# Performance work log

Measured on AMD Instinct MI355X. Metric: run time of the kernel, lower is better.

Reference implementation:

```python
import jax, jax.numpy as jnp
import numpy as np

N = 10000       # nodes (= number of eigenpairs)
NFEAT = 512
NCLASS = 64     # hidden size of attention/FFN when norm='none'
HID = 128       # feat_encoder hidden
DIM = 32        # eig encoder hidden_dim
K = 10          # outer loop count of ParamNonHarmonicEncoding
NF = DIM // 2   # num_freq = 16
OMEGA = 50.0
DMIN = 0.25
NLAYER = 1


def _ln(x, g, b, eps=1e-5):
    m = jnp.mean(x, axis=-1, keepdims=True)
    v = jnp.mean((x - m) ** 2, axis=-1, keepdims=True)
    return g * (x - m) / jnp.sqrt(v + eps) + b


def setup_inputs() -> dict:
    key = jax.random.key(0)
    ks = jax.random.split(key, 32)
    f32 = jnp.float32
    def w(k, shape, s=0.05):
        return jax.random.normal(k, shape, dtype=f32) * s
    inp = {
        "e": jax.random.uniform(ks[0], (N,), dtype=f32),
        "u": jax.random.normal(ks[1], (N, N), dtype=f32) / np.float32(np.sqrt(N)),
        "x": jax.random.normal(ks[2], (N, NFEAT), dtype=f32),
        # feat_encoder: Linear(nfeat,hid) -> ReLU -> Linear(hid,nclass)
        "fe_w1": w(ks[3], (NFEAT, HID)), "fe_b1": jnp.zeros((HID,), f32),
        "fe_w2": w(ks[4], (HID, NCLASS)), "fe_b2": jnp.zeros((NCLASS,), f32),
        # ParamNonHarmonicEncoding
        "freq_deltas": jax.random.uniform(ks[5], (NF,), dtype=f32) * 0.5,
        "freq_bias": jnp.zeros((), f32),
        "readout_w": w(ks[6], (K, 1 + 2 * NF), 0.1),
        "readout_b": jnp.zeros((K,), f32),
        "alpha_w": w(ks[7], (K, 1), 0.3),   # nn.Linear(k,1,bias=False)
        # mha pre-norm
        "mha_ln_g": jnp.ones((NCLASS,), f32), "mha_ln_b": jnp.zeros((NCLASS,), f32),
        # Diff attention (H=1, hidden=nclass)
        "wq1": w(ks[8], (NCLASS, NCLASS)), "bq1": jnp.zeros((NCLASS,), f32),
        "wk1": w(ks[9], (NCLASS, NCLASS)), "bk1": jnp.zeros((NCLASS,), f32),
        "wq2": w(ks[10], (NCLASS, NCLASS)), "bq2": jnp.zeros((NCLASS,), f32),
        "wk2": w(ks[11], (NCLASS, NCLASS)), "bk2": jnp.zeros((NCLASS,), f32),
        "wv": w(ks[12], (NCLASS, NCLASS)), "bv": jnp.zeros((NCLASS,), f32),
        "lq1": w(ks[13], (NCLASS,), 0.1), "lk1": w(ks[14], (NCLASS,), 0.1),
        "lq2": w(ks[15], (NCLASS,), 0.1), "lk2": w(ks[16], (NCLASS,), 0.1),
        "attn_ln_g": jnp.ones((NCLASS,), f32), "attn_ln_b": jnp.zeros((NCLASS,), f32),
        "out_w": w(ks[17], (NCLASS, NCLASS)), "out_b": jnp.zeros((NCLASS,), f32),
        # gating
        "gate_ln_g": jnp.ones((3 * NCLASS,), f32), "gate_ln_b": jnp.zeros((3 * NCLASS,), f32),
        "gate_w": w(ks[18], (3 * NCLASS, 3)), "gate_b": jnp.zeros((3,), f32),
        # FFN
        "ffn_ln_g": jnp.ones((NCLASS,), f32), "ffn_ln_b": jnp.zeros((NCLASS,), f32),
        "ffn_w1": w(ks[19], (NCLASS, NCLASS)), "ffn_b1": jnp.zeros((NCLASS,), f32),
        "ffn_w2": w(ks[20], (NCLASS, NCLASS)), "ffn_b2": jnp.zeros((NCLASS,), f32),
    }
    return inp


def reference(e, u, x, fe_w1, fe_b1, fe_w2, fe_b2,
              freq_deltas, freq_bias, readout_w, readout_b, alpha_w,
              mha_ln_g, mha_ln_b,
              wq1, bq1, wk1, bk1, wq2, bq2, wk2, bk2, wv, bv,
              lq1, lk1, lq2, lk2, attn_ln_g, attn_ln_b, out_w, out_b,
              gate_ln_g, gate_ln_b, gate_w, gate_b,
              ffn_ln_g, ffn_ln_b, ffn_w1, ffn_b1, ffn_w2, ffn_b2):
    # feat encoder (all dropouts are 0 / eval mode)
    h = jnp.maximum(x @ fe_w1 + fe_b1, 0.0) @ fe_w2 + fe_b2          # [N, C]

    # ParamNonHarmonicEncoding, vectorized over the k powers
    deltas = jax.nn.softplus(freq_deltas) + DMIN
    freqs = jnp.cumsum(deltas) + freq_bias
    freqs = OMEGA * jnp.tanh(freqs / OMEGA)                           # [F]
    powers = e[:, None] ** jnp.arange(1, K + 1, dtype=e.dtype)        # [N, K]
    phase = powers[:, :, None] * freqs                                # [N, K, F]
    ns = jnp.asarray(NF ** 0.5, e.dtype)
    feat = jnp.concatenate(
        [jnp.ones_like(powers)[..., None], jnp.sin(phase) / ns, jnp.cos(phase) / ns],
        axis=-1)                                                      # [N, K, 1+2F]
    eig = jnp.einsum('nkf,kf->nk', feat, readout_w) + readout_b      # [N, K]
    new_e = eig @ alpha_w                                             # [N, 1]

    for layer in range(NLAYER):
        # spectral propagation: u @ diag-like(new_e) @ u^T @ h
        utx = u.T @ h                                                 # [N, C]
        h_fur = u @ (new_e * utx)                                     # [N, C]

        # differential linear attention
        mh = _ln(h, mha_ln_g, mha_ln_b)
        q1 = mh @ wq1 + bq1; k1 = mh @ wk1 + bk1
        q2 = mh @ wq2 + bq2; k2 = mh @ wk2 + bk2
        v = mh @ wv + bv
        k1v = k1.T @ v                                                # [C, C]
        k2v = k2.T @ v
        lam1 = jnp.exp(jnp.sum(lq1 * lk1))
        lam2 = jnp.exp(jnp.sum(lq2 * lk2))
        lam_init = 0.8 - 0.6 * float(np.exp(-0.3 * layer))
        lam_full = lam1 - lam2 + lam_init
        xa = q1 @ k1v - (q2 @ k2v) * lam_full
        xa = _ln(xa, attn_ln_g, attn_ln_b) * (1.0 - lam_init)
        mha_h = xa @ out_w + out_b                                    # [N, C]

        # gated mixing
        cat = jnp.concatenate([h, mha_h, h_fur], axis=-1)             # [N, 3C]
        g = jax.nn.softmax(_ln(cat, gate_ln_g, gate_ln_b) @ gate_w + gate_b, axis=-1)
        mix = h * g[:, 0:1] + mha_h * g[:, 1:2] + h_fur * g[:, 2:3]

        f = _ln(mix, ffn_ln_g, ffn_ln_b)
        f = jax.nn.gelu(f @ ffn_w1 + ffn_b1, approximate=False) @ ffn_w2 + ffn_b2
        h = mix + f
    return h
```

## Files before the change

### kernel.cpp

```cpp
#include <hip/hip_runtime.h>
#include <hip/hip_bf16.h>
#include <math.h>

#define NN 10000
#define J48 10048
#define CHUNKS 157
#define CPS 20
#define SPLITS 8

typedef __bf16 bf16;
typedef bf16 bf16x8 __attribute__((ext_vector_type(8)));
typedef float f32x4 __attribute__((ext_vector_type(4)));

__device__ __forceinline__ float wave_sum64(float v) {
#pragma unroll
  for (int m = 32; m >= 1; m >>= 1) v += __shfl_xor(v, m, 64);
  return v;
}

__global__ void prep_kernel(const float* __restrict__ w1, const float* __restrict__ w2,
                            const float* __restrict__ wq1, const float* __restrict__ wk1,
                            const float* __restrict__ wq2, const float* __restrict__ wk2,
                            const float* __restrict__ wvw,
                            const float* __restrict__ bq1, const float* __restrict__ bk1,
                            const float* __restrict__ bq2, const float* __restrict__ bk2,
                            const float* __restrict__ bvv,
                            const float* __restrict__ lq1, const float* __restrict__ lk1,
                            const float* __restrict__ lq2, const float* __restrict__ lk2,
                            const float* __restrict__ freq_deltas, const float* __restrict__ freq_bias,
                            bf16* __restrict__ w1T, bf16* __restrict__ w2T, bf16* __restrict__ qkvT,
                            float* __restrict__ bqkv, float* __restrict__ freqs, float* __restrict__ lamb) {
  int tid = blockIdx.x * blockDim.x + threadIdx.x;
  int nthr = gridDim.x * blockDim.x;
  for (int i = tid; i < 512 * 128; i += nthr) {
    int o = i >> 9, k = i & 511;
    w1T[i] = (bf16)w1[k * 128 + o];
  }
  for (int i = tid; i < 64 * 128; i += nthr) {
    int o = i >> 7, k = i & 127;
    w2T[i] = (bf16)w2[k * 64 + o];
  }
  for (int i = tid; i < 320 * 64; i += nthr) {
    int r = i >> 6, k = i & 63;
    const float* W = (r < 64) ? wq1 : (r < 128) ? wk1 : (r < 192) ? wq2 : (r < 256) ? wk2 : wvw;
    qkvT[i] = (bf16)W[k * 64 + (r & 63)];
  }
  for (int i = tid; i < 320; i += nthr) {
    const float* B = (i < 64) ? bq1 : (i < 128) ? bk1 : (i < 192) ? bq2 : (i < 256) ? bk2 : bvv;
    bqkv[i] = B[i & 63];
  }
  if (blockIdx.x == 0) {
    if (threadIdx.x == 0) {
      float acc = freq_bias[0];
      for (int f = 0; f < 16; f++) {
        acc += log1pf(expf(freq_deltas[f])) + 0.25f;
        freqs[f] = 50.0f * tanhf(acc * (1.0f / 50.0f));
      }
    }
    if (threadIdx.x >= 64 && threadIdx.x < 128) {
      int l = threadIdx.x - 64;
      float s1 = wave_sum64(lq1[l] * lk1[l]);
      float s2 = wave_sum64(lq2[l] * lk2[l]);
      if (l == 0) lamb[0] = expf(s1) - expf(s2) + 0.2f;
    }
  }
}

__global__ void newe_kernel(const float* __restrict__ e, const float* __restrict__ rw,
                            const float* __restrict__ rb, const float* __restrict__ aw,
                            const float* __restrict__ freqs, float* __restrict__ newe) {
  int n = blockIdx.x * blockDim.x + threadIdx.x;
  if (n >= NN) return;
  float fr[16];
#pragma unroll
  for (int f = 0; f < 16; f++) fr[f] = freqs[f];
  float ev = e[n], p = 1.0f, acc = 0.0f;
  for (int k = 0; k < 10; k++) {
    p *= ev;
    float s = rb[k] + rw[k * 33];
#pragma unroll
    for (int f = 0; f < 16; f++) {
      float ph = p * fr[f];
      s += 0.25f * (__sinf(ph) * rw[k * 33 + 1 + f] + __cosf(ph) * rw[k * 33 + 17 + f]);
    }
    acc += s * aw[k];
  }
  newe[n] = acc;
}

__global__ __launch_bounds__(256) void ucopy_kernel(const float* __restrict__ u, bf16* __restrict__ ubf) {
  size_t base = ((size_t)blockIdx.x * 256 + threadIdx.x) * 8;
  size_t stride = (size_t)gridDim.x * 256 * 8;
  for (size_t i = base; i < (size_t)NN * NN; i += stride) {
    float4 a = *(const float4*)(u + i);
    float4 b = *(const float4*)(u + i + 4);
    union { uint4 v; bf16 h[8]; } pk;
    pk.h[0] = (bf16)a.x; pk.h[1] = (bf16)a.y; pk.h[2] = (bf16)a.z; pk.h[3] = (bf16)a.w;
    pk.h[4] = (bf16)b.x; pk.h[5] = (bf16)b.y; pk.h[6] = (bf16)b.z; pk.h[7] = (bf16)b.w;
    *(uint4*)(ubf + i) = pk.v;
  }
}

__global__ __launch_bounds__(256) void g1_kernel(const float* __restrict__ x, const bf16* __restrict__ w1T,
                                                 const float* __restrict__ b1, bf16* __restrict__ t1b) {
  __shared__ bf16 la[64][40];
  __shared__ bf16 lb[128][40];
  const int bm = blockIdx.x * 64;
  const int lane = threadIdx.x & 63, wvid = threadIdx.x >> 6;
  const int am = threadIdx.x >> 2, aseg = (threadIdx.x & 3) * 8;
  const int arow = bm + am;
  f32x4 acc[8] = {};
  float4 aLo, aHi;
  uint4 bChunk[2];
  auto fetchAll = [&](int k0) {
    if (arow < NN) {
      const float4* p = (const float4*)(x + (size_t)arow * 512 + k0 + aseg);
      aLo = p[0]; aHi = p[1];
    } else {
      aLo = make_float4(0.f, 0.f, 0.f, 0.f); aHi = aLo;
    }
#pragma unroll
    for (int r = 0; r < 2; r++) {
      int slot = threadIdx.x * 2 + r;
      int n = slot >> 2, seg = (slot & 3) * 8;
      bChunk[r] = *(const uint4*)(w1T + n * 512 + k0 + seg);
    }
  };
  auto store = [&]() {
    union { uint4 v; bf16 b[8]; } pk;
    float av[8] = {aLo.x, aLo.y, aLo.z, aLo.w, aHi.x, aHi.y, aHi.z, aHi.w};
#pragma unroll
    for (int t = 0; t < 8; t++) pk.b[t] = (bf16)av[t];
    *(uint4*)&la[am][aseg] = pk.v;
#pragma unroll
    for (int r = 0; r < 2; r++) {
      int slot = threadIdx.x * 2 + r;
      int n = slot >> 2, seg = (slot & 3) * 8;
      *(uint4*)&lb[n][seg] = bChunk[r];
    }
  };
  fetchAll(0);
  for (int k0 = 0; k0 < 512; k0 += 32) {
    store();
    if (k0 + 32 < 512) fetchAll(k0 + 32);
    __syncthreads();
    bf16x8 af = *(const bf16x8*)&la[wvid * 16 + (lane & 15)][(lane >> 4) * 8];
#pragma unroll
    for (int s = 0; s < 8; s++) {
      bf16x8 bfr = *(const bf16x8*)&lb[s * 16 + (lane & 15)][(lane >> 4) * 8];
      acc[s] = __builtin_amdgcn_mfma_f32_16x16x32_bf16(af, bfr, acc[s], 0, 0, 0);
    }
    __syncthreads();
  }
#pragma unroll
  for (int s = 0; s < 8; s++) {
    int col = s * 16 + (lane & 15);
    float bvv = b1[col];
#pragma unroll
    for (int r = 0; r < 4; r++) {
      int row = bm + wvid * 16 + (lane >> 4) * 4 + r;
      if (row < NN) {
        float v = acc[s][r] + bvv;
        t1b[(size_t)row * 128 + col] = (bf16)(v > 0.f ? v : 0.f);
      }
    }
  }
}

__global__ __launch_bounds__(256) void g2_kernel(const bf16* __restrict__ t1b, const bf16* __restrict__ w2T,
                                                 const float* __restrict__ b2, const float* __restrict__ lng,
                                                 const float* __restrict__ lnb, float* __restrict__ h,
                                                 bf16* __restrict__ hT, bf16* __restrict__ mh) {
  __shared__ bf16 la[64][72];
  __shared__ bf16 lb[64][72];
  const int bm = blockIdx.x * 64;
  const int lane = threadIdx.x & 63, wvid = threadIdx.x >> 6;
  f32x4 acc[4] = {};
  for (int k0 = 0; k0 < 128; k0 += 64) {
#pragma unroll
    for (int r = 0; r < 2; r++) {
      int slot = threadIdx.x * 2 + r;
      int m = slot >> 3, seg = (slot & 7) * 8;
      int row = bm + m;
      uint4 val = make_uint4(0u, 0u, 0u, 0u);
      if (row < NN) val = *(const uint4*)(t1b + (size_t)row * 128 + k0 + seg);
      *(uint4*)&la[m][seg] = val;
      *(uint4*)&lb[m][seg] = *(const uint4*)(w2T + m * 128 + k0 + seg);
    }
    __syncthreads();
#pragma unroll
    for (int ks = 0; ks < 2; ks++) {
      bf16x8 af = *(const bf16x8*)&la[wvid * 16 + (lane & 15)][ks * 32 + (lane >> 4) * 8];
#pragma unroll
      for (int s = 0; s < 4; s++) {
        bf16x8 bfr = *(const bf16x8*)&lb[s * 16 + (lane & 15)][ks * 32 + (lane >> 4) * 8];
        acc[s] = __builtin_amdgcn_mfma_f32_16x16x32_bf16(af, bfr, acc[s], 0, 0, 0);
      }
    }
    __syncthreads();
  }
  float bv4[4], g4[4], lb4[4];
#pragma unroll
  for (int s = 0; s < 4; s++) {
    int col = s * 16 + (lane & 15);
    bv4[s] = b2[col]; g4[s] = lng[col]; lb4[s] = lnb[col];
  }
#pragma unroll
  for (int r = 0; r < 4; r++) {
    float vals[4], psum = 0.f;
#pragma unroll
    for (int s = 0; s < 4; s++) { vals[s] = acc[s][r] + bv4[s]; psum += vals[s]; }
#pragma unroll
    for (int msk = 1; msk < 16; msk <<= 1) psum += __shfl_xor(psum, msk, 64);
    float mean = psum * (1.0f / 64.0f);
    float pvar = 0.f;
#pragma unroll
    for (int s = 0; s < 4; s++) { float dd = vals[s] - mean; pvar += dd * dd; }
#pragma unroll
    for (int msk = 1; msk < 16; msk <<= 1) pvar += __shfl_xor(pvar, msk, 64);
    float rsq = rsqrtf(pvar * (1.0f / 64.0f) + 1e-5f);
    int row = bm + wvid * 16 + (lane >> 4) * 4 + r;
    if (row < NN) {
#pragma unroll
      for (int s = 0; s < 4; s++) {
        int col = s * 16 + (lane & 15);
        float v = vals[s];
        h[(size_t)row * 64 + col] = v;
        hT[(size_t)col * NN + row] = (bf16)v;
        mh[(size_t)row * 64 + col] = (bf16)(g4[s] * (v - mean) * rsq + lb4[s]);
      }
    }
  }
}

__global__ __launch_bounds__(256) void qkv_kernel(const bf16* __restrict__ mh, const bf16* __restrict__ qkvT,
                                                  const float* __restrict__ bqkv,
                                                  bf16* __restrict__ qq, bf16* __restrict__ kv) {
  __shared__ bf16 la[64][72];
  __shared__ bf16 lb[320][72];
  const int bm = blockIdx.x * 64;
  const int lane = threadIdx.x & 63, wvid = threadIdx.x >> 6;
#pragma unroll
  for (int r = 0; r < 2; r++) {
    int slot = threadIdx.x * 2 + r;
    int m = slot >> 3, seg = (slot & 7) * 8;
    int row = bm + m;
    uint4 val = make_uint4(0u, 0u, 0u, 0u);
    if (row < NN) val = *(const uint4*)(mh + (size_t)row * 64 + seg);
    *(uint4*)&la[m][seg] = val;
  }
#pragma unroll
  for (int r = 0; r < 10; r++) {
    int slot = threadIdx.x * 10 + r;
    int n = slot >> 3, seg = (slot & 7) * 8;
    *(uint4*)&lb[n][seg] = *(const uint4*)(qkvT + n * 64 + seg);
  }
  __syncthreads();
  f32x4 acc[20] = {};
#pragma unroll
  for (int ks = 0; ks < 2; ks++) {
    bf16x8 af = *(const bf16x8*)&la[wvid * 16 + (lane & 15)][ks * 32 + (lane >> 4) * 8];
#pragma unroll
    for (int s = 0; s < 20; s++) {
      bf16x8 bfr = *(const bf16x8*)&lb[s * 16 + (lane & 15)][ks * 32 + (lane >> 4) * 8];
      acc[s] = __builtin_amdgcn_mfma_f32_16x16x32_bf16(af, bfr, acc[s], 0, 0, 0);
    }
  }
#pragma unroll
  for (int s = 0; s < 20; s++) {
    int col = s * 16 + (lane & 15);
    float bvv = bqkv[col];
    bf16* dst; int dc, stride;
    if (col < 64)       { dst = qq; dc = col;       stride = 128; }
    else if (col < 128) { dst = kv; dc = col - 64;  stride = 192; }
    else if (col < 192) { dst = qq; dc = col - 64;  stride = 128; }
    else                { dst = kv; dc = col - 128; stride = 192; }
#pragma unroll
    for (int r = 0; r < 4; r++) {
      int row = bm + wvid * 16 + (lane >> 4) * 4 + r;
      if (row < NN) dst[(size_t)row * stride + dc] = (bf16)(acc[s][r] + bvv);
    }
  }
}

__global__ __launch_bounds__(256) void r1_kernel(const bf16* __restrict__ kv, float* __restrict__ part) {
  int b = blockIdx.x;
  int c1 = threadIdx.x & 63, grp = threadIdx.x >> 6;
  int r0 = b * 16;
  float a1[16] = {}, a2[16] = {};
  for (int r = 0; r < 16; r++) {
    const bf16* rowp = kv + (size_t)(r0 + r) * 192;
    float k1 = (float)rowp[c1];
    float k2 = (float)rowp[64 + c1];
    union { uint4 v; bf16 b[8]; } v0, v1;
    v0.v = *(const uint4*)(rowp + 128 + grp * 16);
    v1.v = *(const uint4*)(rowp + 136 + grp * 16);
#pragma unroll
    for (int q = 0; q < 8; q++) {
      float va = (float)v0.b[q], vb = (float)v1.b[q];
      a1[q] += k1 * va; a2[q] += k2 * va;
      a1[8 + q] += k1 * vb; a2[8 + q] += k2 * vb;
    }
  }
  float* p1 = part + (size_t)b * 8192 + (size_t)c1 * 64 + grp * 16;
  float* p2 = p1 + 4096;
#pragma unroll
  for (int q = 0; q < 16; q++) { p1[q] = a1[q]; p2[q] = a2[q]; }
}

__global__ __launch_bounds__(256) void r2a_kernel(const float* __restrict__ part, float* __restrict__ part2) {
  int flat = blockIdx.x * 256 + threadIdx.x;
  int y = blockIdx.y;
  int b0 = y * 79, b1 = min(625, b0 + 79);
  float s = 0.f;
  for (int b = b0; b < b1; b++) s += part[(size_t)b * 8192 + flat];
  part2[(size_t)flat * 8 + y] = s;
}

__global__ void r2b_kernel(const float* __restrict__ part2, const float* __restrict__ lamb, bf16* __restrict__ Bt) {
  int flat = blockIdx.x * 256 + threadIdx.x;
  int mat = flat >> 12, rem = flat & 4095;
  int d = rem >> 6, c = rem & 63;
  f32x4 lo = *(const f32x4*)(part2 + (size_t)flat * 8);
  f32x4 hi = *(const f32x4*)(part2 + (size_t)flat * 8 + 4);
  float s = lo[0] + lo[1] + lo[2] + lo[3] + hi[0] + hi[1] + hi[2] + hi[3];
  float v = mat ? (-lamb[0] * s) : s;
  Bt[c * 128 + mat * 64 + d] = (bf16)v;
}

__global__ __launch_bounds__(256) void d_split_kernel(const bf16* __restrict__ ubf, const bf16* __restrict__ hT,
                                                      float* __restrict__ dpart) {
  __shared__ bf16 la[64][72];
  __shared__ bf16 lb[64][72];
  const int j0 = blockIdx.x * 64;
  const int sk = blockIdx.y;
  const int c0 = sk * CPS, c1e = min(CHUNKS, c0 + CPS);
  const int t = threadIdx.x;
  const int lane = t & 63, wv = t >> 6;
  const int jl = (t & 15) * 4;
  const int ir = (t >> 4) * 4;
  f32x4 acc[4] = {};
  uint4 aC[2];
  uint2 uc[4];
  auto fetchAll = [&](int i0) {
#pragma unroll
    for (int r = 0; r < 2; r++) {
      int slot = t * 2 + r;
      int c = slot >> 3, seg = (slot & 7) * 8;
      int i = i0 + seg;
      if (i + 7 < NN) aC[r] = *(const uint4*)(hT + (size_t)c * NN + i);
      else {
        union { uint4 v; bf16 b[8]; } tu;
#pragma unroll
        for (int q = 0; q < 8; q++) tu.b[q] = (i + q < NN) ? hT[(size_t)c * NN + i + q] : (bf16)0.f;
        aC[r] = tu.v;
      }
    }
#pragma unroll
    for (int q = 0; q < 4; q++) {
      int i = i0 + ir + q;
      if (i < NN && (j0 + jl + 3) < NN) uc[q] = *(const uint2*)(ubf + (size_t)i * NN + j0 + jl);
      else if (i < NN) {
        union { uint2 w; bf16 b[4]; } tu;
#pragma unroll
        for (int q2 = 0; q2 < 4; q2++) tu.b[q2] = (j0 + jl + q2 < NN) ? ubf[(size_t)i * NN + j0 + jl + q2] : (bf16)0.f;
        uc[q] = tu.w;
      } else uc[q] = make_uint2(0u, 0u);
    }
  };
  auto storeAll = [&]() {
#pragma unroll
    for (int r = 0; r < 2; r++) {
      int slot = t * 2 + r;
      int c = slot >> 3, seg = (slot & 7) * 8;
      *(uint4*)&la[c][seg] = aC[r];
    }
#pragma unroll
    for (int q2 = 0; q2 < 4; q2++) {
      int j = jl + q2;
      int isw = ir ^ (((j >> 2) & 3) << 3);
      union { uint2 w; bf16 b[4]; } pk;
      pk.b[0] = ((const bf16*)&uc[0])[q2];
      pk.b[1] = ((const bf16*)&uc[1])[q2];
      pk.b[2] = ((const bf16*)&uc[2])[q2];
      pk.b[3] = ((const bf16*)&uc[3])[q2];
      *(uint2*)&lb[j][isw] = pk.w;
    }
  };
  fetchAll(c0 * 64);
  for (int ch = c0; ch < c1e; ch++) {
    storeAll();
    if (ch + 1 < c1e) fetchAll((ch + 1) * 64);
    __syncthreads();
#pragma unroll
    for (int ks = 0; ks < 2; ks++) {
      bf16x8 af = *(const bf16x8*)&la[wv * 16 + (lane & 15)][ks * 32 + (lane >> 4) * 8];
#pragma unroll
      for (int s = 0; s < 4; s++) {
        int j = s * 16 + (lane & 15);
        int ioff = (ks * 32 + (lane >> 4) * 8) ^ (((j >> 2) & 3) << 3);
        bf16x8 bfr = *(const bf16x8*)&lb[j][ioff];
        acc[s] = __builtin_amdgcn_mfma_f32_16x16x32_bf16(af, bfr, acc[s], 0, 0, 0);
      }
    }
    __syncthreads();
  }
#pragma unroll
  for (int s = 0; s < 4; s++) {
    int j = j0 + s * 16 + (lane & 15);
#pragma unroll
    for (int r = 0; r < 4; r++) {
      int c = wv * 16 + (lane >> 4) * 4 + r;
      dpart[((size_t)sk * 64 + c) * J48 + j] = acc[s][r];
    }
  }
}

__global__ void dred_kernel(const float* __restrict__ dpart, const float* __restrict__ newe,
                            bf16* __restrict__ wutxT) {
  int idx = blockIdx.x * 256 + threadIdx.x;
  int c = idx / 2512;
  int j = (idx - c * 2512) * 4;
  if (c >= 64 || j >= NN) return;
  f32x4 s = {};
  for (int sk = 0; sk < SPLITS; sk++)
    s += *(const f32x4*)(dpart + ((size_t)sk * 64 + c) * J48 + j);
  union { uint2 w; bf16 b[4]; } pk;
#pragma unroll
  for (int q = 0; q < 4; q++) pk.b[q] = (bf16)(newe[j + q] * s[q]);
  *(uint2*)&wutxT[(size_t)c * NN + j] = pk.w;
}

__global__ __launch_bounds__(256) void e_split_kernel(const bf16* __restrict__ ubf, const bf16* __restrict__ wutxT,
                                                      float* __restrict__ epart) {
  __shared__ bf16 la[64][72];
  __shared__ bf16 lb[64][72];
  const int bm = blockIdx.x * 64;
  const int sk = blockIdx.y;
  const int c0 = sk * CPS, c1e = min(CHUNKS, c0 + CPS);
  const int t = threadIdx.x;
  const int lane = t & 63, wv = t >> 6;
  const int mA = t >> 2, segA = (t & 3) * 16;
  const int mrow = bm + mA;
  f32x4 acc[4] = {};
  uint4 aU[2];
  uint4 bC[2];
  auto fetchAll = [&](int j0) {
    int j = j0 + segA;
    if (mrow < NN && j + 15 < NN) {
      aU[0] = *(const uint4*)(ubf + (size_t)mrow * NN + j);
      aU[1] = *(const uint4*)(ubf + (size_t)mrow * NN + j + 8);
    } else {
      union { uint4 v[2]; bf16 b[16]; } tu;
#pragma unroll
      for (int q = 0; q < 16; q++)
        tu.b[q] = (mrow < NN && j + q < NN) ? ubf[(size_t)mrow * NN + j + q] : (bf16)0.f;
      aU[0] = tu.v[0]; aU[1] = tu.v[1];
    }
#pragma unroll
    for (int r = 0; r < 2; r++) {
      int slot = t * 2 + r;
      int c = slot >> 3, seg = (slot & 7) * 8;
      int jj = j0 + seg;
      if (jj + 7 < NN) bC[r] = *(const uint4*)(wutxT + (size_t)c * NN + jj);
      else {
        union { uint4 v; bf16 b[8]; } tu;
#pragma unroll
        for (int q = 0; q < 8; q++) tu.b[q] = (jj + q < NN) ? wutxT[(size_t)c * NN + jj + q] : (bf16)0.f;
        bC[r] = tu.v;
      }
    }
  };
  auto storeAll = [&]() {
    *(uint4*)&la[mA][segA] = aU[0];
    *(uint4*)&la[mA][segA + 8] = aU[1];
#pragma unroll
    for (int r = 0; r < 2; r++) {
      int slot = t * 2 + r;
      int c = slot >> 3, seg = (slot & 7) * 8;
      *(uint4*)&lb[c][seg] = bC[r];
    }
  };
  fetchAll(c0 * 64);
  for (int ch = c0; ch < c1e; ch++) {
    storeAll();
    if (ch + 1 < c1e) fetchAll((ch + 1) * 64);
    __syncthreads();
#pragma unroll
    for (int ks = 0; ks < 2; ks++) {
      bf16x8 af = *(const bf16x8*)&la[wv * 16 + (lane & 15)][ks * 32 + (lane >> 4) * 8];
#pragma unroll
      for (int s = 0; s < 4; s++) {
        bf16x8 bfr = *(const bf16x8*)&lb[s * 16 + (lane & 15)][ks * 32 + (lane >> 4) * 8];
        acc[s] = __builtin_amdgcn_mfma_f32_16x16x32_bf16(af, bfr, acc[s], 0, 0, 0);
      }
    }
    __syncthreads();
  }
#pragma unroll
  for (int s = 0; s < 4; s++) {
    int col = s * 16 + (lane & 15);
#pragma unroll
    for (int r = 0; r < 4; r++) {
      int row = wv * 16 + (lane >> 4) * 4 + r;
      epart[((size_t)sk * J48 + bm + row) * 64 + col] = acc[s][r];
    }
  }
}

__global__ void ered_kernel(const float* __restrict__ epart, float* __restrict__ h_fur) {
  int idx = blockIdx.x * 256 + threadIdx.x;
  if (idx >= NN * 16) return;
  size_t off = (size_t)idx * 4;
  f32x4 s = {};
  for (int sk = 0; sk < SPLITS; sk++)
    s += *(const f32x4*)(epart + (size_t)sk * (J48 * 64) + off);
  *(f32x4*)(h_fur + off) = s;
}

__global__ __launch_bounds__(256) void hattn_kernel(const bf16* __restrict__ qq, const bf16* __restrict__ Bt,
                                                    const float* __restrict__ g, const float* __restrict__ b,
                                                    bf16* __restrict__ xan) {
  __shared__ bf16 la[64][136];
  __shared__ bf16 lb[64][136];
  const int bm = blockIdx.x * 64;
  const int lane = threadIdx.x & 63, wvid = threadIdx.x >> 6;
#pragma unroll
  for (int r = 0; r < 4; r++) {
    int slot = threadIdx.x * 4 + r;
    int m = slot >> 4, seg = (slot & 15) * 8;
    int row = bm + m;
    uint4 val = make_uint4(0u, 0u, 0u, 0u);
    if (row < NN) val = *(const uint4*)(qq + (size_t)row * 128 + seg);
    *(uint4*)&la[m][seg] = val;
    *(uint4*)&lb[m][seg] = *(const uint4*)(Bt + m * 128 + seg);
  }
  __syncthreads();
  f32x4 acc[4] = {};
#pragma unroll
  for (int ks = 0; ks < 4; ks++) {
    bf16x8 af = *(const bf16x8*)&la[wvid * 16 + (lane & 15)][ks * 32 + (lane >> 4) * 8];
#pragma unroll
    for (int s = 0; s < 4; s++) {
      bf16x8 bfr = *(const bf16x8*)&lb[s * 16 + (lane & 15)][ks * 32 + (lane >> 4) * 8];
      acc[s] = __builtin_amdgcn_mfma_f32_16x16x32_bf16(af, bfr, acc[s], 0, 0, 0);
    }
  }
#pragma unroll
  for (int r = 0; r < 4; r++) {
    float psum = acc[0][r] + acc[1][r] + acc[2][r] + acc[3][r];
#pragma unroll
    for (int msk = 1; msk < 16; msk <<= 1) psum += __shfl_xor(psum, msk, 64);
    float mean = psum * (1.0f / 64.0f);
    float pvar = 0.f;
#pragma unroll
    for (int s = 0; s < 4; s++) { float dd = acc[s][r] - mean; pvar += dd * dd; }
#pragma unroll
    for (int msk = 1; msk < 16; msk <<= 1) pvar += __shfl_xor(pvar, msk, 64);
    float rsq = rsqrtf(pvar * (1.0f / 64.0f) + 1e-5f);
    int row = bm + wvid * 16 + (lane >> 4) * 4 + r;
    if (row < NN) {
#pragma unroll
      for (int s = 0; s < 4; s++) {
        int col = s * 16 + (lane & 15);
        float o = 0.8f * (g[col] * (acc[s][r] - mean) * rsq + b[col]);
        xan[(size_t)row * 64 + col] = (bf16)o;
      }
    }
  }
}

__global__ __launch_bounds__(256) void final_kernel(const float* __restrict__ h, const float* __restrict__ h_fur,
                                                    const bf16* __restrict__ xan,
                                                    const float* __restrict__ out_w, const float* __restrict__ out_b,
                                                    const float* __restrict__ gg, const float* __restrict__ gb,
                                                    const float* __restrict__ gw, const float* __restrict__ gbias,
                                                    const float* __restrict__ fg, const float* __restrict__ fb,
                                                    const float* __restrict__ fw1, const float* __restrict__ fb1,
                                                    const float* __restrict__ fw2, const float* __restrict__ fb2,
                                                    float* __restrict__ out) {
  __shared__ float s_ow[64][64];
  __shared__ float s_w1[64][64];
  __shared__ float s_w2[64][64];
  __shared__ float s_gw[192][3];
  __shared__ float s_row[4][64];
  const int lane = threadIdx.x & 63, wvid = threadIdx.x >> 6;
  for (int i = threadIdx.x; i < 4096; i += 256) {
    ((float*)s_ow)[i] = out_w[i];
    ((float*)s_w1)[i] = fw1[i];
    ((float*)s_w2)[i] = fw2[i];
  }
  for (int i = threadIdx.x; i < 576; i += 256) ((float*)s_gw)[i] = gw[i];
  const int row = blockIdx.x * 4 + wvid;
  float x_h = h[(size_t)row * 64 + lane];
  float x_f = h_fur[(size_t)row * 64 + lane];
  float x_a = (float)xan[(size_t)row * 64 + lane];
  s_row[wvid][lane] = x_a;
  __syncthreads();
  float mha = out_b[lane];
#pragma unroll 8
  for (int d = 0; d < 64; d++) mha += s_row[wvid][d] * s_ow[d][lane];
  float m3 = wave_sum64(x_h + mha + x_f) * (1.0f / 192.0f);
  float dh = x_h - m3, dm = mha - m3, df = x_f - m3;
  float v3 = wave_sum64(dh * dh + dm * dm + df * df) * (1.0f / 192.0f);
  float rs3 = rsqrtf(v3 + 1e-5f);
  float l0 = gg[lane] * dh * rs3 + gb[lane];
  float l1 = gg[64 + lane] * dm * rs3 + gb[64 + lane];
  float l2 = gg[128 + lane] * df * rs3 + gb[128 + lane];
  float p0 = l0 * s_gw[lane][0] + l1 * s_gw[64 + lane][0] + l2 * s_gw[128 + lane][0];
  float p1 = l0 * s_gw[lane][1] + l1 * s_gw[64 + lane][1] + l2 * s_gw[128 + lane][1];
  float p2 = l0 * s_gw[lane][2] + l1 * s_gw[64 + lane][2] + l2 * s_gw[128 + lane][2];
  p0 = wave_sum64(p0) + gbias[0];
  p1 = wave_sum64(p1) + gbias[1];
  p2 = wave_sum64(p2) + gbias[2];
  float mx = fmaxf(p0, fmaxf(p1, p2));
  float e0 = expf(p0 - mx), e1 = expf(p1 - mx), e2 = expf(p2 - mx);
  float inv = 1.0f / (e0 + e1 + e2);
  float mix = x_h * (e0 * inv) + mha * (e1 * inv) + x_f * (e2 * inv);
  float mf = wave_sum64(mix) * (1.0f / 64.0f);
  float dmx = mix - mf;
  float vf = wave_sum64(dmx * dmx) * (1.0f / 64.0f);
  float f = fg[lane] * dmx * rsqrtf(vf + 1e-5f) + fb[lane];
  __syncthreads();
  s_row[wvid][lane] = f;
  __syncthreads();
  float t1 = fb1[lane];
#pragma unroll 8
  for (int d = 0; d < 64; d++) t1 += s_row[wvid][d] * s_w1[d][lane];
  t1 = 0.5f * t1 * (1.0f + erff(t1 * 0.70710678118654752f));
  __syncthreads();
  s_row[wvid][lane] = t1;
  __syncthreads();
  float f2 = fb2[lane];
#pragma unroll 8
  for (int d = 0; d < 64; d++) f2 += s_row[wvid][d] * s_w2[d][lane];
  out[(size_t)row * 64 + lane] = mix + f2;
}

extern "C" void kernel_launch(void* const* d_in, const int* in_sizes, int n_in,
                              void* d_out, int out_size, void* d_ws, size_t ws_size,
                              hipStream_t stream) {
  const float* e          = (const float*)d_in[0];
  const float* u          = (const float*)d_in[1];
  const float* x          = (const float*)d_in[2];
  const float* fe_w1      = (const float*)d_in[3];
  const float* fe_b1      = (const float*)d_in[4];
  const float* fe_w2      = (const float*)d_in[5];
  const float* fe_b2      = (const float*)d_in[6];
  const float* freq_deltas= (const float*)d_in[7];
  const float* freq_bias  = (const float*)d_in[8];
  const float* readout_w  = (const float*)d_in[9];
  const float* readout_b  = (const float*)d_in[10];
  const float* alpha_w    = (const float*)d_in[11];
  const float* mha_ln_g   = (const float*)d_in[12];
  const float* mha_ln_b   = (const float*)d_in[13];
  const float* wq1        = (const float*)d_in[14];
  const float* bq1        = (const float*)d_in[15];
  const float* wk1        = (const float*)d_in[16];
  const float* bk1        = (const float*)d_in[17];
  const float* wq2        = (const float*)d_in[18];
  const float* bq2        = (const float*)d_in[19];
  const float* wk2        = (const float*)d_in[20];
  const float* bk2        = (const float*)d_in[21];
  const float* wv_in      = (const float*)d_in[22];
  const float* bv_in      = (const float*)d_in[23];
  const float* lq1        = (const float*)d_in[24];
  const float* lk1        = (const float*)d_in[25];
  const float* lq2        = (const float*)d_in[26];
  const float* lk2        = (const float*)d_in[27];
  const float* attn_ln_g  = (const float*)d_in[28];
  const float* attn_ln_b  = (const float*)d_in[29];
  const float* out_w      = (const float*)d_in[30];
  const float* out_b      = (const float*)d_in[31];
  const float* gate_ln_g  = (const float*)d_in[32];
  const float* gate_ln_b  = (const float*)d_in[33];
  const float* gate_w     = (const float*)d_in[34];
  const float* gate_b     = (const float*)d_in[35];
  const float* ffn_ln_g   = (const float*)d_in[36];
  const float* ffn_ln_b   = (const float*)d_in[37];
  const float* ffn_w1     = (const float*)d_in[38];
  const float* ffn_b1     = (const float*)d_in[39];
  const float* ffn_w2     = (const float*)d_in[40];
  const float* ffn_b2     = (const float*)d_in[41];

  constexpr size_t OFF_H     = 0;
  constexpr size_t OFF_T1B   = 2560000;
  constexpr size_t OFF_HT    = 5120000;
  constexpr size_t OFF_MH    = 6400000;
  constexpr size_t OFF_QQ    = 7680000;
  constexpr size_t OFF_KV    = 10240000;
  constexpr size_t OFF_WUTXT = 14080000;
  constexpr size_t OFF_HFUR  = 15360000;
  constexpr size_t OFF_XAN   = 17920000;
  constexpr size_t OFF_NEWE  = 19200000;
  constexpr size_t OFF_BT    = 19240064;
  constexpr size_t OFF_W1T   = 19256448;
  constexpr size_t OFF_W2T   = 19387520;
  constexpr size_t OFF_QKVT  = 19403904;
  constexpr size_t OFF_BQKV  = 19444864;
  constexpr size_t OFF_FREQS = 19446144;
  constexpr size_t OFF_LAM   = 19446208;
  constexpr size_t OFF_BIG   = 19446272;
  constexpr size_t SZ_SPART  = (size_t)SPLITS * 64 * J48 * 4;
  constexpr size_t OFF_PART2 = OFF_BIG + SZ_SPART;
  constexpr size_t OFF_UBF   = OFF_PART2 + 262144;
  constexpr size_t WS_NEED   = OFF_UBF + (size_t)NN * NN * 2;
  if (ws_size < WS_NEED) return;

  char* ws = (char*)d_ws;
  float* h_buf   = (float*)(ws + OFF_H);
  bf16*  t1b     = (bf16*)(ws + OFF_T1B);
  bf16*  hT      = (bf16*)(ws + OFF_HT);
  bf16*  mh      = (bf16*)(ws + OFF_MH);
  bf16*  qq      = (bf16*)(ws + OFF_QQ);
  bf16*  kv      = (bf16*)(ws + OFF_KV);
  bf16*  wutxT   = (bf16*)(ws + OFF_WUTXT);
  float* h_fur   = (float*)(ws + OFF_HFUR);
  bf16*  xan     = (bf16*)(ws + OFF_XAN);
  float* newe    = (float*)(ws + OFF_NEWE);
  bf16*  Bt      = (bf16*)(ws + OFF_BT);
  bf16*  w1T     = (bf16*)(ws + OFF_W1T);
  bf16*  w2T     = (bf16*)(ws + OFF_W2T);
  bf16*  qkvT    = (bf16*)(ws + OFF_QKVT);
  float* bqkv    = (float*)(ws + OFF_BQKV);
  float* freqs   = (float*)(ws + OFF_FREQS);
  float* lamb    = (float*)(ws + OFF_LAM);
  float* part    = (float*)(ws + OFF_BIG);
  float* part2   = (float*)(ws + OFF_PART2);
  float* dpart   = (float*)(ws + OFF_BIG);
  float* epart   = (float*)(ws + OFF_BIG);
  bf16*  ubf     = (bf16*)(ws + OFF_UBF);

  prep_kernel<<<64, 256, 0, stream>>>(fe_w1, fe_w2, wq1, wk1, wq2, wk2, wv_in,
                                      bq1, bk1, bq2, bk2, bv_in,
                                      lq1, lk1, lq2, lk2, freq_deltas, freq_bias,
                                      w1T, w2T, qkvT, bqkv, freqs, lamb);
  newe_kernel<<<40, 256, 0, stream>>>(e, readout_w, readout_b, alpha_w, freqs, newe);
  g1_kernel<<<157, 256, 0, stream>>>(x, w1T, fe_b1, t1b);
  g2_kernel<<<157, 256, 0, stream>>>(t1b, w2T, fe_b2, mha_ln_g, mha_ln_b, h_buf, hT, mh);
  qkv_kernel<<<157, 256, 0, stream>>>(mh, qkvT, bqkv, qq, kv);
  r1_kernel<<<625, 256, 0, stream>>>(kv, part);
  r2a_kernel<<<dim3(32, 8), 256, 0, stream>>>(part, part2);
  r2b_kernel<<<32, 256, 0, stream>>>(part2, lamb, Bt);
  ucopy_kernel<<<2048, 256, 0, stream>>>(u, ubf);
  d_split_kernel<<<dim3(157, SPLITS), 256, 0, stream>>>(ubf, hT, dpart);
  dred_kernel<<<628, 256, 0, stream>>>(dpart, newe, wutxT);
  e_split_kernel<<<dim3(157, SPLITS), 256, 0, stream>>>(ubf, wutxT, epart);
  ered_kernel<<<625, 256, 0, stream>>>(epart, h_fur);
  hattn_kernel<<<157, 256, 0, stream>>>(qq, Bt, attn_ln_g, attn_ln_b, xan);
  final_kernel<<<2500, 256, 0, stream>>>(h_buf, h_fur, xan, out_w, out_b,
                                         gate_ln_g, gate_ln_b, gate_w, gate_b,
                                         ffn_ln_g, ffn_ln_b, ffn_w1, ffn_b1, ffn_w2, ffn_b2,
                                         (float*)d_out);
}
```

Baseline: 405.5 us.

## Fuse fp32-to-bf16 conversion of u into split GEMM loads and relax barriers

Removes the separate pass that converts the 10000x10000 eigenvector matrix to bf16. The two split GEMM kernels now read fp32 u directly and convert it while staging to LDS. This removes one full write plus reread of the bf16 copy and one launch, but doubles the bytes each GEMM reads. The block barriers now wait only on LDS counters, so global prefetches can stay in flight across the barrier.

```diff
diff --git a/kernel.cpp b/kernel.cpp
--- a/kernel.cpp
+++ b/kernel.cpp
@@ -11,6 +11,13 @@
 typedef __bf16 bf16;
 typedef bf16 bf16x8 __attribute__((ext_vector_type(8)));
 typedef float f32x4 __attribute__((ext_vector_type(4)));
+
+#define SYNC_LDS() do {                                      \
+    asm volatile("s_waitcnt lgkmcnt(0)" ::: "memory");       \
+    __builtin_amdgcn_sched_barrier(0);                       \
+    __builtin_amdgcn_s_barrier();                            \
+    __builtin_amdgcn_sched_barrier(0);                       \
+  } while (0)
 
 __device__ __forceinline__ float wave_sum64(float v) {
 #pragma unroll
@@ -88,19 +95,6 @@
   newe[n] = acc;
 }
 
-__global__ __launch_bounds__(256) void ucopy_kernel(const float* __restrict__ u, bf16* __restrict__ ubf) {
-  size_t base = ((size_t)blockIdx.x * 256 + threadIdx.x) * 8;
-  size_t stride = (size_t)gridDim.x * 256 * 8;
-  for (size_t i = base; i < (size_t)NN * NN; i += stride) {
-    float4 a = *(const float4*)(u + i);
-    float4 b = *(const float4*)(u + i + 4);
-    union { uint4 v; bf16 h[8]; } pk;
-    pk.h[0] = (bf16)a.x; pk.h[1] = (bf16)a.y; pk.h[2] = (bf16)a.z; pk.h[3] = (bf16)a.w;
-    pk.h[4] = (bf16)b.x; pk.h[5] = (bf16)b.y; pk.h[6] = (bf16)b.z; pk.h[7] = (bf16)b.w;
-    *(uint4*)(ubf + i) = pk.v;
-  }
-}
-
 __global__ __launch_bounds__(256) void g1_kernel(const float* __restrict__ x, const bf16* __restrict__ w1T,
                                                  const float* __restrict__ b1, bf16* __restrict__ t1b) {
   __shared__ bf16 la[64][40];
@@ -328,7 +322,7 @@
   Bt[c * 128 + mat * 64 + d] = (bf16)v;
 }
 
-__global__ __launch_bounds__(256) void d_split_kernel(const bf16* __restrict__ ubf, const bf16* __restrict__ hT,
+__global__ __launch_bounds__(256) void d_split_kernel(const float* __restrict__ u, const bf16* __restrict__ hT,
                                                       float* __restrict__ dpart) {
   __shared__ bf16 la[64][72];
   __shared__ bf16 lb[64][72];
@@ -341,7 +335,7 @@
   const int ir = (t >> 4) * 4;
   f32x4 acc[4] = {};
   uint4 aC[2];
-  uint2 uc[4];
+  float4 bC[4];
   auto fetchAll = [&](int i0) {
 #pragma unroll
     for (int r = 0; r < 2; r++) {
@@ -359,13 +353,13 @@
 #pragma unroll
     for (int q = 0; q < 4; q++) {
       int i = i0 + ir + q;
-      if (i < NN && (j0 + jl + 3) < NN) uc[q] = *(const uint2*)(ubf + (size_t)i * NN + j0 + jl);
+      if (i < NN && (j0 + jl + 3) < NN) bC[q] = *(const float4*)(u + (size_t)i * NN + j0 + jl);
       else if (i < NN) {
-        union { uint2 w; bf16 b[4]; } tu;
-#pragma unroll
-        for (int q2 = 0; q2 < 4; q2++) tu.b[q2] = (j0 + jl + q2 < NN) ? ubf[(size_t)i * NN + j0 + jl + q2] : (bf16)0.f;
-        uc[q] = tu.w;
-      } else uc[q] = make_uint2(0u, 0u);
+        float tmp[4];
+#pragma unroll
+        for (int q2 = 0; q2 < 4; q2++) tmp[q2] = (j0 + jl + q2 < NN) ? u[(size_t)i * NN + j0 + jl + q2] : 0.f;
+        bC[q] = make_float4(tmp[0], tmp[1], tmp[2], tmp[3]);
+      } else bC[q] = make_float4(0.f, 0.f, 0.f, 0.f);
     }
   };
   auto storeAll = [&]() {
@@ -380,10 +374,10 @@
       int j = jl + q2;
       int isw = ir ^ (((j >> 2) & 3) << 3);
       union { uint2 w; bf16 b[4]; } pk;
-      pk.b[0] = ((const bf16*)&uc[0])[q2];
-      pk.b[1] = ((const bf16*)&uc[1])[q2];
-      pk.b[2] = ((const bf16*)&uc[2])[q2];
-      pk.b[3] = ((const bf16*)&uc[3])[q2];
+      pk.b[0] = (bf16)((float*)&bC[0])[q2];
+      pk.b[1] = (bf16)((float*)&bC[1])[q2];
+      pk.b[2] = (bf16)((float*)&bC[2])[q2];
+      pk.b[3] = (bf16)((float*)&bC[3])[q2];
       *(uint2*)&lb[j][isw] = pk.w;
     }
   };
@@ -391,7 +385,7 @@
   for (int ch = c0; ch < c1e; ch++) {
     storeAll();
     if (ch + 1 < c1e) fetchAll((ch + 1) * 64);
-    __syncthreads();
+    SYNC_LDS();
 #pragma unroll
     for (int ks = 0; ks < 2; ks++) {
       bf16x8 af = *(const bf16x8*)&la[wv * 16 + (lane & 15)][ks * 32 + (lane >> 4) * 8];
@@ -403,7 +397,7 @@
         acc[s] = __builtin_amdgcn_mfma_f32_16x16x32_bf16(af, bfr, acc[s], 0, 0, 0);
       }
     }
-    __syncthreads();
+    SYNC_LDS();
   }
 #pragma unroll
   for (int s = 0; s < 4; s++) {
@@ -431,7 +425,7 @@
   *(uint2*)&wutxT[(size_t)c * NN + j] = pk.w;
 }
 
-__global__ __launch_bounds__(256) void e_split_kernel(const bf16* __restrict__ ubf, const bf16* __restrict__ wutxT,
+__global__ __launch_bounds__(256) void e_split_kernel(const float* __restrict__ u, const bf16* __restrict__ wutxT,
                                                       float* __restrict__ epart) {
   __shared__ bf16 la[64][72];
   __shared__ bf16 lb[64][72];
@@ -443,19 +437,24 @@
   const int mA = t >> 2, segA = (t & 3) * 16;
   const int mrow = bm + mA;
   f32x4 acc[4] = {};
-  uint4 aU[2];
+  float4 aC[4];
   uint4 bC[2];
   auto fetchAll = [&](int j0) {
     int j = j0 + segA;
     if (mrow < NN && j + 15 < NN) {
-      aU[0] = *(const uint4*)(ubf + (size_t)mrow * NN + j);
-      aU[1] = *(const uint4*)(ubf + (size_t)mrow * NN + j + 8);
+      const float4* p = (const float4*)(u + (size_t)mrow * NN + j);
+      aC[0] = p[0]; aC[1] = p[1]; aC[2] = p[2]; aC[3] = p[3];
     } else {
-      union { uint4 v[2]; bf16 b[16]; } tu;
-#pragma unroll
-      for (int q = 0; q < 16; q++)
-        tu.b[q] = (mrow < NN && j + q < NN) ? ubf[(size_t)mrow * NN + j + q] : (bf16)0.f;
-      aU[0] = tu.v[0]; aU[1] = tu.v[1];
+#pragma unroll
+      for (int q = 0; q < 4; q++) {
+        float tmp[4];
+#pragma unroll
+        for (int q2 = 0; q2 < 4; q2++) {
+          int jj = j + q * 4 + q2;
+          tmp[q2] = (mrow < NN && jj < NN) ? u[(size_t)mrow * NN + jj] : 0.f;
+        }
+        aC[q] = make_float4(tmp[0], tmp[1], tmp[2], tmp[3]);
+      }
     }
 #pragma unroll
     for (int r = 0; r < 2; r++) {
@@ -472,8 +471,13 @@
     }
   };
   auto storeAll = [&]() {
-    *(uint4*)&la[mA][segA] = aU[0];
-    *(uint4*)&la[mA][segA + 8] = aU[1];
+    union { uint4 v[2]; bf16 b[16]; } pk;
+#pragma unroll
+    for (int q = 0; q < 4; q++)
+#pragma unroll
+      for (int q2 = 0; q2 < 4; q2++) pk.b[q * 4 + q2] = (bf16)((float*)&aC[q])[q2];
+    *(uint4*)&la[mA][segA] = pk.v[0];
+    *(uint4*)&la[mA][segA + 8] = pk.v[1];
 #pragma unroll
     for (int r = 0; r < 2; r++) {
       int slot = t * 2 + r;
@@ -485,7 +489,7 @@
   for (int ch = c0; ch < c1e; ch++) {
     storeAll();
     if (ch + 1 < c1e) fetchAll((ch + 1) * 64);
-    __syncthreads();
+    SYNC_LDS();
 #pragma unroll
     for (int ks = 0; ks < 2; ks++) {
       bf16x8 af = *(const bf16x8*)&la[wv * 16 + (lane & 15)][ks * 32 + (lane >> 4) * 8];
@@ -495,7 +499,7 @@
         acc[s] = __builtin_amdgcn_mfma_f32_16x16x32_bf16(af, bfr, acc[s], 0, 0, 0);
       }
     }
-    __syncthreads();
+    SYNC_LDS();
   }
 #pragma unroll
   for (int s = 0; s < 4; s++) {
@@ -703,8 +707,7 @@
   constexpr size_t OFF_BIG   = 19446272;
   constexpr size_t SZ_SPART  = (size_t)SPLITS * 64 * J48 * 4;
   constexpr size_t OFF_PART2 = OFF_BIG + SZ_SPART;
-  constexpr size_t OFF_UBF   = OFF_PART2 + 262144;
-  constexpr size_t WS_NEED   = OFF_UBF + (size_t)NN * NN * 2;
+  constexpr size_t WS_NEED   = OFF_PART2 + 262144;
   if (ws_size < WS_NEED) return;
 
   char* ws = (char*)d_ws;
@@ -729,7 +732,6 @@
   float* part2   = (float*)(ws + OFF_PART2);
   float* dpart   = (float*)(ws + OFF_BIG);
   float* epart   = (float*)(ws + OFF_BIG);
-  bf16*  ubf     = (bf16*)(ws + OFF_UBF);
 
   prep_kernel<<<64, 256, 0, stream>>>(fe_w1, fe_w2, wq1, wk1, wq2, wk2, wv_in,
                                       bq1, bk1, bq2, bk2, bv_in,
@@ -742,10 +744,9 @@
   r1_kernel<<<625, 256, 0, stream>>>(kv, part);
   r2a_kernel<<<dim3(32, 8), 256, 0, stream>>>(part, part2);
   r2b_kernel<<<32, 256, 0, stream>>>(part2, lamb, Bt);
-  ucopy_kernel<<<2048, 256, 0, stream>>>(u, ubf);
-  d_split_kernel<<<dim3(157, SPLITS), 256, 0, stream>>>(ubf, hT, dpart);
+  d_split_kernel<<<dim3(157, SPLITS), 256, 0, stream>>>(u, hT, dpart);
   dred_kernel<<<628, 256, 0, stream>>>(dpart, newe, wutxT);
-  e_split_kernel<<<dim3(157, SPLITS), 256, 0, stream>>>(ubf, wutxT, epart);
+  e_split_kernel<<<dim3(157, SPLITS), 256, 0, stream>>>(u, wutxT, epart);
   ered_kernel<<<625, 256, 0, stream>>>(epart, h_fur);
   hattn_kernel<<<157, 256, 0, stream>>>(qq, Bt, attn_ln_g, attn_ln_b, xan);
   final_kernel<<<2500, 256, 0, stream>>>(h_buf, h_fur, xan, out_w, out_b,
```

Measured after the change: 361.1 us. 10.9% less time.
